# Optimization experiments

Hardware: AMD Instinct MI355X
Metric: run time of the kernel (lower is better)

Reference implementation:

```python
import jax, jax.numpy as jnp
import numpy as np
import math

N_NEURONS = 2048
TAU_MEM = 10.0
TAU_SYN = 5.0
V_TH = 1.0
V_RESET = 0.0
ALPHA_MEM = math.exp(-1.0 / TAU_MEM)
ALPHA_SYN = math.exp(-1.0 / TAU_SYN)


def setup_inputs() -> dict:
    key = jax.random.key(0)
    B, T, N = 8, 1024, N_NEURONS
    x = jax.random.normal(key, (B, T, N), dtype=jnp.float32)
    membrane = jnp.zeros((B, N), dtype=jnp.float32)
    trace = jnp.zeros((B, N), dtype=jnp.float32)
    return {"x": x, "membrane": membrane, "trace": trace}


def reference(x, membrane, trace):
    """StatefulLIF.forward_sequence: LIF recurrence over T via lax.scan.

    x: [B, T, N]; membrane, trace: [B, N].
    Returns (spikes [B, T, N], final_membrane [B, N], final_trace [B, N]).
    """
    a_m = jnp.asarray(ALPHA_MEM, x.dtype)
    a_s = jnp.asarray(ALPHA_SYN, x.dtype)
    reset_amt = jnp.asarray(V_TH - V_RESET, x.dtype)

    def step(carry, x_t):
        m, tr = carry
        m = a_m * m + (1 - a_m) * x_t
        s = (m > V_TH).astype(x_t.dtype)  # Heaviside spike
        m = m - reset_amt * s
        tr = a_s * tr + s
        return (m, tr), s

    # scan over time: move T to leading axis
    (m_f, tr_f), spikes_t = jax.lax.scan(step, (membrane, trace), jnp.swapaxes(x, 0, 1))
    spikes = jnp.swapaxes(spikes_t, 0, 1)  # [B, T, N]
    return spikes, m_f, tr_f
```

## Files before the change

### kernel.cpp

```cpp
#include <hip/hip_runtime.h>


#define LIF_B 8
#define LIF_T 1024
#define LIF_N 2048

#define A_MEM 0.90483741803595952f
#define A_SYN 0.81873075307798185f

#define CHUNK 64
#define NCHUNK (LIF_T / CHUNK)
#define NBUF 4
#define LPC 16

#define BARRIER()                                  \
  do {                                             \
    __asm__ __volatile__("" ::: "memory");         \
    __builtin_amdgcn_s_barrier();                  \
    __asm__ __volatile__("" ::: "memory");         \
  } while (0)

#define WAITV(n) __asm__ __volatile__("s_waitcnt vmcnt(" #n ")" ::: "memory")

__global__ __launch_bounds__(128) void lif_pc_kernel(
    const float* __restrict__ x,
    const float* __restrict__ m0,
    const float* __restrict__ tr0,
    float* __restrict__ out) {
  __shared__ float xbuf[NBUF][CHUNK][64];

  const int wid = threadIdx.x >> 6;
  const int l   = threadIdx.x & 63;
  const int b   = blockIdx.x >> 5;
  const int n0  = (blockIdx.x * 64) & (LIF_N - 1);
  const size_t plane = (size_t)LIF_T * LIF_N;

  const float* __restrict__ gl =
      x + (size_t)b * plane + (size_t)(l >> 4) * LIF_N + n0 + 4 * (l & 15);

  #define ISSUE_CHUNK(cc)                                                    \
    do {                                                                     \
      const float* g_ = gl + (size_t)(cc) * CHUNK * LIF_N;                   \
      float(*lb_)[64] = xbuf[(cc) & (NBUF - 1)];                             \
      _Pragma("unroll")                                                      \
      for (int i_ = 0; i_ < LPC; ++i_) {                                     \
        __builtin_amdgcn_global_load_lds(                                    \
            (const __attribute__((address_space(1))) void*)(                 \
                g_ + (size_t)(4 * i_) * LIF_N),                              \
            (__attribute__((address_space(3))) void*)(&lb_[4 * i_][0]),      \
            16, 0, 0);                                                       \
      }                                                                      \
    } while (0)

  float m = 0.f, tr = 0.f;
  float* sp = nullptr;
  if (wid == 0) {
    ISSUE_CHUNK(0);
    ISSUE_CHUNK(1);
    ISSUE_CHUNK(2);
    WAITV(32);
  } else {
    const int chain = blockIdx.x * 64 + l;
    m  = m0[chain];
    tr = tr0[chain];
    sp = out + (size_t)b * plane + n0 + l;
  }

  BARRIER();

  constexpr float am   = A_MEM;
  constexpr float as   = A_SYN;
  constexpr float onem = 1.0f - A_MEM;

  #pragma unroll 1
  for (int c = 0; c < NCHUNK; ++c) {
    if (wid == 0) {
      if (c + 3 < NCHUNK) {
        ISSUE_CHUNK(c + 3);
        WAITV(32);
      } else if (c == NCHUNK - 3) {
        WAITV(16);
      } else if (c == NCHUNK - 2) {
        WAITV(0);
      }
    } else {
      float xr[CHUNK];
      float(*lb)[64] = xbuf[c & (NBUF - 1)];
      #pragma unroll
      for (int j = 0; j < CHUNK; ++j) xr[j] = lb[j][l];
      float* spc = sp + (size_t)c * CHUNK * LIF_N;
      #pragma unroll
      for (int j = 0; j < CHUNK; ++j) {
        m = fmaf(am, m, onem * xr[j]);
        float s_ = (m > 1.0f) ? 1.0f : 0.0f;
        m -= s_;
        tr = fmaf(as, tr, s_);
        __builtin_nontemporal_store(s_, spc + (size_t)j * LIF_N);
      }
    }
    BARRIER();
  }
  #undef ISSUE_CHUNK

  if (wid == 1) {
    const int chain = blockIdx.x * 64 + l;
    float* mf  = out + (size_t)LIF_B * plane;
    float* trf = mf + (size_t)LIF_B * LIF_N;
    mf[chain]  = m;
    trf[chain] = tr;
  }
}

extern "C" void kernel_launch(void* const* d_in, const int* in_sizes, int n_in,
                              void* d_out, int out_size, void* d_ws, size_t ws_size,
                              hipStream_t stream) {
  const float* x   = (const float*)d_in[0];
  const float* m0  = (const float*)d_in[1];
  const float* tr0 = (const float*)d_in[2];
  float* out = (float*)d_out;

  const int grid = (LIF_B * LIF_N) / 64;
  lif_pc_kernel<<<grid, 128, 0, stream>>>(x, m0, tr0, out);
}
```

Measured before the change: 123.4 us.

## Stage spike outputs through LDS and store via dedicated vectorized writer waves

```diff
diff --git a/kernel.cpp b/kernel.cpp
--- a/kernel.cpp
+++ b/kernel.cpp
@@ -10,8 +10,11 @@
 
 #define CHUNK 64
 #define NCHUNK (LIF_T / CHUNK)
-#define NBUF 4
+#define NXBUF 4
+#define NSBUF 2
 #define LPC 16
+
+typedef float f32x4 __attribute__((ext_vector_type(4)));
 
 #define BARRIER()                                  \
   do {                                             \
@@ -21,13 +24,15 @@
   } while (0)
 
 #define WAITV(n) __asm__ __volatile__("s_waitcnt vmcnt(" #n ")" ::: "memory")
+#define WAITL0() __asm__ __volatile__("s_waitcnt lgkmcnt(0)" ::: "memory")
 
-__global__ __launch_bounds__(128) void lif_pc_kernel(
+__global__ __launch_bounds__(256) void lif_pc_kernel(
     const float* __restrict__ x,
     const float* __restrict__ m0,
     const float* __restrict__ tr0,
     float* __restrict__ out) {
-  __shared__ float xbuf[NBUF][CHUNK][64];
+  __shared__ float xbuf[NXBUF][CHUNK][64];
+  __shared__ float sbuf[NSBUF][CHUNK][64];
 
   const int wid = threadIdx.x >> 6;
   const int l   = threadIdx.x & 63;
@@ -41,7 +46,7 @@
   #define ISSUE_CHUNK(cc)                                                    \
     do {                                                                     \
       const float* g_ = gl + (size_t)(cc) * CHUNK * LIF_N;                   \
-      float(*lb_)[64] = xbuf[(cc) & (NBUF - 1)];                             \
+      float(*lb_)[64] = xbuf[(cc) & (NXBUF - 1)];                            \
       _Pragma("unroll")                                                      \
       for (int i_ = 0; i_ < LPC; ++i_) {                                     \
         __builtin_amdgcn_global_load_lds(                                    \
@@ -53,17 +58,15 @@
     } while (0)
 
   float m = 0.f, tr = 0.f;
-  float* sp = nullptr;
   if (wid == 0) {
     ISSUE_CHUNK(0);
     ISSUE_CHUNK(1);
     ISSUE_CHUNK(2);
     WAITV(32);
-  } else {
+  } else if (wid == 1) {
     const int chain = blockIdx.x * 64 + l;
     m  = m0[chain];
     tr = tr0[chain];
-    sp = out + (size_t)b * plane + n0 + l;
   }
 
   BARRIER();
@@ -73,7 +76,7 @@
   constexpr float onem = 1.0f - A_MEM;
 
   #pragma unroll 1
-  for (int c = 0; c < NCHUNK; ++c) {
+  for (int c = 0; c <= NCHUNK; ++c) {
     if (wid == 0) {
       if (c + 3 < NCHUNK) {
         ISSUE_CHUNK(c + 3);
@@ -83,19 +86,43 @@
       } else if (c == NCHUNK - 2) {
         WAITV(0);
       }
+    } else if (wid == 1) {
+      if (c < NCHUNK) {
+        float xr[CHUNK];
+        float(*lb)[64] = xbuf[c & (NXBUF - 1)];
+        #pragma unroll
+        for (int j = 0; j < CHUNK; ++j) xr[j] = lb[j][l];
+        float(*sb)[64] = sbuf[c & (NSBUF - 1)];
+        #pragma unroll
+        for (int j = 0; j < CHUNK; ++j) {
+          m = fmaf(am, m, onem * xr[j]);
+          float md = m - 1.0f;
+          bool  gt = (m > 1.0f);
+          float s_ = gt ? 1.0f : 0.0f;
+          m = gt ? md : m;
+          tr = fmaf(as, tr, s_);
+          sb[j][l] = s_;
+        }
+        WAITL0();
+      }
     } else {
-      float xr[CHUNK];
-      float(*lb)[64] = xbuf[c & (NBUF - 1)];
-      #pragma unroll
-      for (int j = 0; j < CHUNK; ++j) xr[j] = lb[j][l];
-      float* spc = sp + (size_t)c * CHUNK * LIF_N;
-      #pragma unroll
-      for (int j = 0; j < CHUNK; ++j) {
-        m = fmaf(am, m, onem * xr[j]);
-        float s_ = (m > 1.0f) ? 1.0f : 0.0f;
-        m -= s_;
-        tr = fmaf(as, tr, s_);
-        __builtin_nontemporal_store(s_, spc + (size_t)j * LIF_N);
+      if (c >= 1) {
+        const int w2 = wid - 2;
+        float(*sb)[64] = sbuf[(c - 1) & (NSBUF - 1)];
+        float* g = out + (size_t)b * plane +
+                   ((size_t)(c - 1) * CHUNK + 32 * w2 + (l >> 4)) * LIF_N +
+                   n0 + 4 * (l & 15);
+        f32x4 v[8];
+        #pragma unroll
+        for (int i = 0; i < 8; ++i) {
+          const float* src = &sb[32 * w2 + 4 * i + (l >> 4)][4 * (l & 15)];
+          v[i] = *reinterpret_cast<const f32x4*>(src);
+        }
+        #pragma unroll
+        for (int i = 0; i < 8; ++i) {
+          __builtin_nontemporal_store(
+              v[i], reinterpret_cast<f32x4*>(g + (size_t)(4 * i) * LIF_N));
+        }
       }
     }
     BARRIER();
@@ -120,5 +147,5 @@
   float* out = (float*)d_out;
 
   const int grid = (LIF_B * LIF_N) / 64;
-  lif_pc_kernel<<<grid, 128, 0, stream>>>(x, m0, tr0, out);
+  lif_pc_kernel<<<grid, 256, 0, stream>>>(x, m0, tr0, out);
 }
```

After: 120.4 us. 2.4% less time.
